# Kernel optimization log

Measured on AMD Instinct MI355X. Metric: run time of the kernel, lower is better.

## Reference

```python
import jax, jax.numpy as jnp
import numpy as np

NUM_DAYOFWEEK, NUM_TIME, NUM_MONTH, NUM_DAY = 7, 24, 12, 31
NUM_DESTINATION = 100000
NUM_FACTOR = 128
NUM_DIM = NUM_FACTOR // 4  # 32
N = 1048576


def setup_inputs() -> dict:
    key = jax.random.key(0)
    ks = jax.random.split(key, 10)
    std = 0.1
    return {
        "dayofweek": jax.random.randint(ks[0], (N,), 0, NUM_DAYOFWEEK),
        "time": jax.random.randint(ks[1], (N,), 0, NUM_TIME),
        "month": jax.random.randint(ks[2], (N,), 0, NUM_MONTH),
        "day": jax.random.randint(ks[3], (N,), 0, NUM_DAY),
        "destination": jax.random.randint(ks[4], (N,), 0, NUM_DESTINATION),
        "W_dayofweek": std * jax.random.normal(ks[5], (NUM_DAYOFWEEK, NUM_DIM), dtype=jnp.float32),
        "W_time": std * jax.random.normal(ks[6], (NUM_TIME, NUM_DIM), dtype=jnp.float32),
        "W_month": std * jax.random.normal(ks[7], (NUM_MONTH, NUM_DIM), dtype=jnp.float32),
        "W_day": std * jax.random.normal(ks[8], (NUM_DAY, NUM_DIM), dtype=jnp.float32),
        "W_item": std * jax.random.normal(ks[9], (NUM_DESTINATION, NUM_FACTOR), dtype=jnp.float32),
    }


def reference(dayofweek, time, month, day, destination,
              W_dayofweek, W_time, W_month, W_day, W_item) -> jnp.ndarray:
    # Gather per-feature embeddings and concat into user vector [N, num_factor]
    user = jnp.concatenate([
        W_dayofweek[dayofweek],  # [N, 32]
        W_time[time],            # [N, 32]
        W_month[month],          # [N, 32]
        W_day[day],              # [N, 32]
    ], axis=-1)
    item = W_item[destination]   # [N, 128]
    # Original: diagonal(mm(user, item.T)) == rowwise dot product; compute it directly.
    return jnp.sum(user * item, axis=-1)  # [N]
```

## Files before the change

kernel.cpp:

```cpp
#include <hip/hip_runtime.h>


typedef unsigned long long u64;

constexpr int NDIM = 32;
constexpr int SZ_DOW = 7 * NDIM, SZ_TIM = 24 * NDIM, SZ_MON = 12 * NDIM, SZ_DAY = 31 * NDIM;
constexpr int B_DOW = 0;
constexpr int B_TIM = B_DOW + SZ_DOW;
constexpr int B_MON = B_TIM + SZ_TIM;
constexpr int B_DAY = B_MON + SZ_MON;
constexpr int TAB_TOT = B_DAY + SZ_DAY;

constexpr int NB     = 32;
constexpr int DDIV   = 3125;
constexpr int SLICES = 256;
constexpr int SPB    = 4096;
constexpr int BIN_T  = 1024;
constexpr int IPT    = SPB / BIN_T;

__device__ __forceinline__ unsigned short f2bf(float f) {
    const unsigned u = __float_as_uint(f);
    return (unsigned short)((u + 0x7FFFu + ((u >> 16) & 1u)) >> 16);
}

__device__ __forceinline__ float dot8bf(uint4 a, float4 u0, float4 u1) {
    float s;
    s  = __uint_as_float(a.x << 16)          * u0.x;
    s += __uint_as_float(a.x & 0xFFFF0000u)  * u0.y;
    s += __uint_as_float(a.y << 16)          * u0.z;
    s += __uint_as_float(a.y & 0xFFFF0000u)  * u0.w;
    s += __uint_as_float(a.z << 16)          * u1.x;
    s += __uint_as_float(a.z & 0xFFFF0000u)  * u1.y;
    s += __uint_as_float(a.w << 16)          * u1.z;
    s += __uint_as_float(a.w & 0xFFFF0000u)  * u1.w;
    return s;
}

__device__ __forceinline__ void load_tab(float* tab, const float* Wdow, const float* Wtim,
                                         const float* Wmon, const float* Wday, int nthr) {
    const int t = threadIdx.x;
    for (int i = t; i < SZ_DOW; i += nthr) tab[B_DOW + i] = Wdow[i];
    for (int i = t; i < SZ_TIM; i += nthr) tab[B_TIM + i] = Wtim[i];
    for (int i = t; i < SZ_MON; i += nthr) tab[B_MON + i] = Wmon[i];
    for (int i = t; i < SZ_DAY; i += nthr) tab[B_DAY + i] = Wday[i];
}

__global__ __launch_bounds__(BIN_T)
void prep_kernel(const int* __restrict__ dow, const int* __restrict__ tim,
                 const int* __restrict__ mon, const int* __restrict__ day,
                 const int* __restrict__ dest,
                 int* __restrict__ cntG, int* __restrict__ lbaseG,
                 u64* __restrict__ payload, int n,
                 const float* __restrict__ Witem, unsigned short* __restrict__ Wb,
                 int witem_elems)
{
    __shared__ u64 stage[SPB];
    __shared__ int hist[NB], lbase[NB], cursor[NB];

    const int t = threadIdx.x, b = blockIdx.x;
    const int g0 = b * SPB;
    const int rem = n - g0;
    const int len = rem < SPB ? rem : SPB;

    int dreg[IPT], pkreg[IPT];
#pragma unroll
    for (int i = 0; i < IPT; i++) {
        const int k = i * BIN_T + t;
        if (k < len) {
            const int idx = g0 + k;
            dreg[i]  = dest[idx];
            pkreg[i] = dow[idx] | (tim[idx] << 3) | (mon[idx] << 8) | (day[idx] << 12);
        } else { dreg[i] = -1; pkreg[i] = 0; }
    }

    if (Wb) {
        const int nf4   = witem_elems >> 2;
        const int chunk = (nf4 + SLICES - 1) / SLICES;
        const int c0    = b * chunk;
        const int c1    = min(c0 + chunk, nf4);
        const float4* src = (const float4*)Witem;
        ushort4* dst = (ushort4*)Wb;
        for (int i = c0 + t; i < c1; i += BIN_T) {
            const float4 v = src[i];
            ushort4 o;
            o.x = f2bf(v.x); o.y = f2bf(v.y); o.z = f2bf(v.z); o.w = f2bf(v.w);
            dst[i] = o;
        }
    }

    if (t < NB) hist[t] = 0;
    __syncthreads();
#pragma unroll
    for (int i = 0; i < IPT; i++)
        if (dreg[i] >= 0) atomicAdd(&hist[dreg[i] / DDIV], 1);
    __syncthreads();
    if (t == 0) {
        int run = 0;
        for (int q = 0; q < NB; q++) { lbase[q] = run; run += hist[q]; }
    }
    __syncthreads();
    if (t < NB) { cursor[t] = lbase[t]; cntG[b * NB + t] = hist[t]; lbaseG[b * NB + t] = lbase[t]; }
    __syncthreads();
#pragma unroll
    for (int i = 0; i < IPT; i++) {
        const int k = i * BIN_T + t;
        if (k < len) {
            const int j = atomicAdd(&cursor[dreg[i] / DDIV], 1);
            stage[j] = (u64)(unsigned)(g0 + k)
                     | ((u64)(unsigned)dreg[i]  << 20)
                     | ((u64)(unsigned)pkreg[i] << 37);
        }
    }
    __syncthreads();
#pragma unroll
    for (int i = 0; i < IPT; i++) {
        const int k = i * BIN_T + t;
        if (k < len) payload[g0 + k] = stage[k];
    }
}

__global__ __launch_bounds__(256, 8)
void mf_main_bf16(const u64* __restrict__ payload,
                  const float* __restrict__ Wdow, const float* __restrict__ Wtim,
                  const float* __restrict__ Wmon, const float* __restrict__ Wday,
                  const unsigned short* __restrict__ Wb,
                  const int* __restrict__ cntG, const int* __restrict__ lbaseG,
                  float* __restrict__ out)
{
    __shared__ float tab[TAB_TOT];
    load_tab(tab, Wdow, Wtim, Wmon, Wday, 256);
    __syncthreads();

    const int tid = threadIdx.x;
    const int sub = tid & 63;
    const int wv  = tid >> 6;
    const int g   = sub >> 3;
    const int l8  = sub & 7;
    const int jt   = l8 >> 1;
    const int half = (l8 & 1) * 16;
    const int tbj  = (jt == 0) ? B_DOW : (jt == 1) ? B_TIM : (jt == 2) ? B_MON : B_DAY;
    const int shj  = (jt == 0) ? 37    : (jt == 1) ? 40    : (jt == 2) ? 45    : 49;
    const int mkj  = (jt == 0) ? 7     : (jt == 1) ? 31    : (jt == 2) ? 15    : 31;

    const int x = blockIdx.x & 7;
    const int s = blockIdx.x >> 3;

    for (int p = 0; p < 4; p++) {
        const int q  = x + 8 * p;
        const int L  = cntG[s * NB + q];
        const int st = s * SPB + lbaseG[s * NB + q];

        int i = wv * 16;
        u64 p0 = (i + g < L)     ? payload[st + i + g]     : 0ull;
        u64 p1 = (i + 8 + g < L) ? payload[st + i + 8 + g] : 0ull;

        for (; i < L; i += 64) {
            const bool v0 = (i + g) < L, v1 = (i + 8 + g) < L;
            const u64 c0 = p0, c1 = p1;
            const int ni = i + 64;
            p0 = (ni + g < L)     ? payload[st + ni + g]     : 0ull;
            p1 = (ni + 8 + g < L) ? payload[st + ni + 8 + g] : 0ull;

            const int d0 = (int)((c0 >> 20) & 0x1FFFFull);
            const int d1 = (int)((c1 >> 20) & 0x1FFFFull);

            const uint4* r0 = (const uint4*)(Wb + (long)d0 * 128 + (l8 << 4));
            const uint4* r1 = (const uint4*)(Wb + (long)d1 * 128 + (l8 << 4));
            const uint4 A0 = r0[0], B0 = r0[1];
            const uint4 A1 = r1[0], B1 = r1[1];

            const int ix0 = (int)((c0 >> shj) & (u64)mkj);
            const int ix1 = (int)((c1 >> shj) & (u64)mkj);
            const float* u0p = &tab[tbj + ix0 * NDIM + half];
            const float* u1p = &tab[tbj + ix1 * NDIM + half];
            const float4 u00 = *(const float4*)(u0p);
            const float4 u01 = *(const float4*)(u0p + 4);
            const float4 u02 = *(const float4*)(u0p + 8);
            const float4 u03 = *(const float4*)(u0p + 12);
            const float4 u10 = *(const float4*)(u1p);
            const float4 u11 = *(const float4*)(u1p + 4);
            const float4 u12 = *(const float4*)(u1p + 8);
            const float4 u13 = *(const float4*)(u1p + 12);

            float a0 = dot8bf(A0, u00, u01) + dot8bf(B0, u02, u03);
            float a1 = dot8bf(A1, u10, u11) + dot8bf(B1, u12, u13);

            a0 += __shfl_xor(a0, 1);  a1 += __shfl_xor(a1, 1);
            a0 += __shfl_xor(a0, 2);  a1 += __shfl_xor(a1, 2);
            a0 += __shfl_xor(a0, 4);  a1 += __shfl_xor(a1, 4);

            if (l8 == 0) {
                if (v0) out[(int)(c0 & 0xFFFFFull)] = a0;
                if (v1) out[(int)(c1 & 0xFFFFFull)] = a1;
            }
        }
    }
}

__global__ __launch_bounds__(256, 8)
void mf_main_f32(const u64* __restrict__ payload,
                 const float* __restrict__ Wdow, const float* __restrict__ Wtim,
                 const float* __restrict__ Wmon, const float* __restrict__ Wday,
                 const float* __restrict__ Witem,
                 const int* __restrict__ cntG, const int* __restrict__ lbaseG,
                 float* __restrict__ out)
{
    __shared__ float tab[TAB_TOT];
    load_tab(tab, Wdow, Wtim, Wmon, Wday, 256);
    __syncthreads();
    const int tid = threadIdx.x;
    const int sub = tid & 63;
    const int wv  = tid >> 6;
    const int g   = sub >> 3;
    const int l8  = sub & 7;
    const int col = l8 * 4;
    const int tb[4] = {B_DOW, B_TIM, B_MON, B_DAY};
    const int sh[4] = {37, 40, 45, 49};
    const int mk[4] = {7, 31, 15, 31};
    const int x = blockIdx.x & 7;
    const int s = blockIdx.x >> 3;
    for (int p = 0; p < 4; p++) {
        const int q  = x + 8 * p;
        const int L  = cntG[s * NB + q];
        const int st = s * SPB + lbaseG[s * NB + q];
        for (int i = wv * 16; i < L; i += 64) {
            const int i0 = i + g, i1 = i + 8 + g;
            const bool v0 = i0 < L, v1 = i1 < L;
            const u64 p0 = v0 ? payload[st + i0] : 0ull;
            const u64 p1 = v1 ? payload[st + i1] : 0ull;
            const int d0 = (int)((p0 >> 20) & 0x1FFFFull);
            const int d1 = (int)((p1 >> 20) & 0x1FFFFull);
            const float* r0 = Witem + (long)d0 * 128 + col;
            const float* r1 = Witem + (long)d1 * 128 + col;
            float4 it0[4], it1[4], us0[4], us1[4];
#pragma unroll
            for (int j = 0; j < 4; j++) it0[j] = *reinterpret_cast<const float4*>(r0 + j * NDIM);
#pragma unroll
            for (int j = 0; j < 4; j++) it1[j] = *reinterpret_cast<const float4*>(r1 + j * NDIM);
#pragma unroll
            for (int j = 0; j < 4; j++) {
                const int idx = (int)((p0 >> sh[j]) & (u64)mk[j]);
                us0[j] = *reinterpret_cast<const float4*>(&tab[tb[j] + idx * NDIM + col]);
            }
#pragma unroll
            for (int j = 0; j < 4; j++) {
                const int idx = (int)((p1 >> sh[j]) & (u64)mk[j]);
                us1[j] = *reinterpret_cast<const float4*>(&tab[tb[j] + idx * NDIM + col]);
            }
            float a0 = 0.f, a1 = 0.f;
#pragma unroll
            for (int j = 0; j < 4; j++) {
                a0 += it0[j].x * us0[j].x + it0[j].y * us0[j].y
                    + it0[j].z * us0[j].z + it0[j].w * us0[j].w;
                a1 += it1[j].x * us1[j].x + it1[j].y * us1[j].y
                    + it1[j].z * us1[j].z + it1[j].w * us1[j].w;
            }
            a0 += __shfl_xor(a0, 1);  a1 += __shfl_xor(a1, 1);
            a0 += __shfl_xor(a0, 2);  a1 += __shfl_xor(a1, 2);
            a0 += __shfl_xor(a0, 4);  a1 += __shfl_xor(a1, 4);
            if (l8 == 0) {
                if (v0) out[(int)(p0 & 0xFFFFFull)] = a0;
                if (v1) out[(int)(p1 & 0xFFFFFull)] = a1;
            }
        }
    }
}

__global__ __launch_bounds__(256, 8)
void mf_dot_kernel(const int* __restrict__ dow, const int* __restrict__ tim,
                   const int* __restrict__ mon, const int* __restrict__ day,
                   const int* __restrict__ dest,
                   const float* __restrict__ Wdow, const float* __restrict__ Wtim,
                   const float* __restrict__ Wmon, const float* __restrict__ Wday,
                   const float* __restrict__ Witem,
                   float* __restrict__ out, int n_samples)
{
    __shared__ float tab[TAB_TOT];
    load_tab(tab, Wdow, Wtim, Wmon, Wday, 256);
    __syncthreads();
    const int tid = threadIdx.x;
    const int lane = tid & 63, sub = lane & 31, wave = tid >> 6, half = lane >> 5;
    const int t = sub >> 3, dofs = (sub & 7) * 4;
    const int* idxp  = (t == 0) ? dow   : (t == 1) ? tim   : (t == 2) ? mon   : day;
    const int  tbase = (t == 0) ? B_DOW : (t == 1) ? B_TIM : (t == 2) ? B_MON : B_DAY;
    long n = (long)blockIdx.x * 8 + wave * 2 + half;
    const long stride = (long)gridDim.x * 8;
    for (; n < n_samples; n += stride) {
        const int idx = idxp[n];
        const int ds  = dest[n];
        const float4 u  = *reinterpret_cast<const float4*>(&tab[tbase + idx * NDIM + dofs]);
        const float4 it = *reinterpret_cast<const float4*>(&Witem[(long)ds * 128 + sub * 4]);
        float r = u.x * it.x + u.y * it.y + u.z * it.z + u.w * it.w;
        r += __shfl_xor(r, 16); r += __shfl_xor(r, 8); r += __shfl_xor(r, 4);
        r += __shfl_xor(r, 2);  r += __shfl_xor(r, 1);
        if (sub == 0) out[n] = r;
    }
}

extern "C" void kernel_launch(void* const* d_in, const int* in_sizes, int n_in,
                              void* d_out, int out_size, void* d_ws, size_t ws_size,
                              hipStream_t stream)
{
    const int*   dow   = (const int*)d_in[0];
    const int*   tim   = (const int*)d_in[1];
    const int*   mon   = (const int*)d_in[2];
    const int*   day   = (const int*)d_in[3];
    const int*   dest  = (const int*)d_in[4];
    const float* Wdow  = (const float*)d_in[5];
    const float* Wtim  = (const float*)d_in[6];
    const float* Wmon  = (const float*)d_in[7];
    const float* Wday  = (const float*)d_in[8];
    const float* Witem = (const float*)d_in[9];
    float* out = (float*)d_out;

    const int n  = in_sizes[0];
    const int we = in_sizes[9];
    const int cap = SLICES * SPB;

    const size_t off_wb       = 64 * 1024;
    const size_t off_pay_full = (off_wb + (size_t)we * 2 + 255) & ~(size_t)255;
    const size_t need_full    = off_pay_full + (size_t)cap * 8;
    const size_t off_pay_mid  = 64 * 1024;
    const size_t need_mid     = off_pay_mid + (size_t)cap * 8;

    if ((size_t)ws_size < need_mid || n > cap) {
        hipLaunchKernelGGL(mf_dot_kernel, dim3(2048), dim3(256), 0, stream,
                           dow, tim, mon, day, dest,
                           Wdow, Wtim, Wmon, Wday, Witem, out, n);
        return;
    }

    const bool full = (size_t)ws_size >= need_full;

    int* cntG   = (int*)d_ws;
    int* lbaseG = (int*)((char*)d_ws + 32 * 1024);
    unsigned short* Wb = full ? (unsigned short*)((char*)d_ws + off_wb) : nullptr;
    u64* payload = (u64*)((char*)d_ws + (full ? off_pay_full : off_pay_mid));

    hipLaunchKernelGGL(prep_kernel, dim3(SLICES), dim3(BIN_T), 0, stream,
                       dow, tim, mon, day, dest, cntG, lbaseG, payload, n,
                       Witem, Wb, we);
    if (full)
        hipLaunchKernelGGL(mf_main_bf16, dim3(SLICES * 8), dim3(256), 0, stream,
                           payload, Wdow, Wtim, Wmon, Wday, Wb, cntG, lbaseG, out);
    else
        hipLaunchKernelGGL(mf_main_f32, dim3(SLICES * 8), dim3(256), 0, stream,
                           payload, Wdow, Wtim, Wmon, Wday, Witem, cntG, lbaseG, out);
}
```

Before: 150.9 us.

## Drop bf16 item-table conversion, use fp32 gather with finer destination bins

Removes the per-call conversion of the whole 100000x128 item table to bf16 and reads fp32 item rows directly in the main kernel. That conversion read 51MB and wrote 25MB on every call. The price is doubled bytes per gathered item row. Destination bins go from 32 to 64 for better cache locality of each block's slice of the item table. Other changes: a wave shuffle scan replaces the serial prefix sum, count and base are packed into one int2 read before the table load, and embedding rows are padded to a 36-float stride to spread shared-memory banks.

```diff
diff --git a/kernel.cpp b/kernel.cpp
--- a/kernel.cpp
+++ b/kernel.cpp
@@ -3,59 +3,39 @@
 
 typedef unsigned long long u64;
 
-constexpr int NDIM = 32;
-constexpr int SZ_DOW = 7 * NDIM, SZ_TIM = 24 * NDIM, SZ_MON = 12 * NDIM, SZ_DAY = 31 * NDIM;
+constexpr int NDIM    = 32;
+constexpr int RSTRIDE = 36;
 constexpr int B_DOW = 0;
-constexpr int B_TIM = B_DOW + SZ_DOW;
-constexpr int B_MON = B_TIM + SZ_TIM;
-constexpr int B_DAY = B_MON + SZ_MON;
-constexpr int TAB_TOT = B_DAY + SZ_DAY;
-
-constexpr int NB     = 32;
-constexpr int DDIV   = 3125;
+constexpr int B_TIM = B_DOW + 7  * RSTRIDE;
+constexpr int B_MON = B_TIM + 24 * RSTRIDE;
+constexpr int B_DAY = B_MON + 12 * RSTRIDE;
+constexpr int TAB_TOT = B_DAY + 31 * RSTRIDE;
+
+constexpr int NB     = 64;
+constexpr int DDIV   = 1563;
 constexpr int SLICES = 256;
 constexpr int SPB    = 4096;
 constexpr int BIN_T  = 1024;
 constexpr int IPT    = SPB / BIN_T;
 
-__device__ __forceinline__ unsigned short f2bf(float f) {
-    const unsigned u = __float_as_uint(f);
-    return (unsigned short)((u + 0x7FFFu + ((u >> 16) & 1u)) >> 16);
-}
-
-__device__ __forceinline__ float dot8bf(uint4 a, float4 u0, float4 u1) {
-    float s;
-    s  = __uint_as_float(a.x << 16)          * u0.x;
-    s += __uint_as_float(a.x & 0xFFFF0000u)  * u0.y;
-    s += __uint_as_float(a.y << 16)          * u0.z;
-    s += __uint_as_float(a.y & 0xFFFF0000u)  * u0.w;
-    s += __uint_as_float(a.z << 16)          * u1.x;
-    s += __uint_as_float(a.z & 0xFFFF0000u)  * u1.y;
-    s += __uint_as_float(a.w << 16)          * u1.z;
-    s += __uint_as_float(a.w & 0xFFFF0000u)  * u1.w;
-    return s;
-}
-
 __device__ __forceinline__ void load_tab(float* tab, const float* Wdow, const float* Wtim,
                                          const float* Wmon, const float* Wday, int nthr) {
     const int t = threadIdx.x;
-    for (int i = t; i < SZ_DOW; i += nthr) tab[B_DOW + i] = Wdow[i];
-    for (int i = t; i < SZ_TIM; i += nthr) tab[B_TIM + i] = Wtim[i];
-    for (int i = t; i < SZ_MON; i += nthr) tab[B_MON + i] = Wmon[i];
-    for (int i = t; i < SZ_DAY; i += nthr) tab[B_DAY + i] = Wday[i];
+    for (int i = t; i < 7  * NDIM; i += nthr) tab[B_DOW + (i >> 5) * RSTRIDE + (i & 31)] = Wdow[i];
+    for (int i = t; i < 24 * NDIM; i += nthr) tab[B_TIM + (i >> 5) * RSTRIDE + (i & 31)] = Wtim[i];
+    for (int i = t; i < 12 * NDIM; i += nthr) tab[B_MON + (i >> 5) * RSTRIDE + (i & 31)] = Wmon[i];
+    for (int i = t; i < 31 * NDIM; i += nthr) tab[B_DAY + (i >> 5) * RSTRIDE + (i & 31)] = Wday[i];
 }
 
 __global__ __launch_bounds__(BIN_T)
 void prep_kernel(const int* __restrict__ dow, const int* __restrict__ tim,
                  const int* __restrict__ mon, const int* __restrict__ day,
                  const int* __restrict__ dest,
-                 int* __restrict__ cntG, int* __restrict__ lbaseG,
-                 u64* __restrict__ payload, int n,
-                 const float* __restrict__ Witem, unsigned short* __restrict__ Wb,
-                 int witem_elems)
+                 int2* __restrict__ clG,
+                 u64* __restrict__ payload, int n)
 {
     __shared__ u64 stage[SPB];
-    __shared__ int hist[NB], lbase[NB], cursor[NB];
+    __shared__ int hist[NB], cursor[NB];
 
     const int t = threadIdx.x, b = blockIdx.x;
     const int g0 = b * SPB;
@@ -73,33 +53,23 @@
         } else { dreg[i] = -1; pkreg[i] = 0; }
     }
 
-    if (Wb) {
-        const int nf4   = witem_elems >> 2;
-        const int chunk = (nf4 + SLICES - 1) / SLICES;
-        const int c0    = b * chunk;
-        const int c1    = min(c0 + chunk, nf4);
-        const float4* src = (const float4*)Witem;
-        ushort4* dst = (ushort4*)Wb;
-        for (int i = c0 + t; i < c1; i += BIN_T) {
-            const float4 v = src[i];
-            ushort4 o;
-            o.x = f2bf(v.x); o.y = f2bf(v.y); o.z = f2bf(v.z); o.w = f2bf(v.w);
-            dst[i] = o;
-        }
-    }
-
     if (t < NB) hist[t] = 0;
     __syncthreads();
 #pragma unroll
     for (int i = 0; i < IPT; i++)
         if (dreg[i] >= 0) atomicAdd(&hist[dreg[i] / DDIV], 1);
     __syncthreads();
-    if (t == 0) {
-        int run = 0;
-        for (int q = 0; q < NB; q++) { lbase[q] = run; run += hist[q]; }
-    }
-    __syncthreads();
-    if (t < NB) { cursor[t] = lbase[t]; cntG[b * NB + t] = hist[t]; lbaseG[b * NB + t] = lbase[t]; }
+    if (t < 64) {
+        int v = hist[t];
+#pragma unroll
+        for (int d = 1; d < 64; d <<= 1) {
+            const int nv = __shfl_up(v, d);
+            if (t >= d) v += nv;
+        }
+        const int base = v - hist[t];
+        cursor[t] = base;
+        clG[b * NB + t] = make_int2(hist[t], base);
+    }
     __syncthreads();
 #pragma unroll
     for (int i = 0; i < IPT; i++) {
@@ -119,96 +89,27 @@
     }
 }
 
-__global__ __launch_bounds__(256, 8)
-void mf_main_bf16(const u64* __restrict__ payload,
-                  const float* __restrict__ Wdow, const float* __restrict__ Wtim,
-                  const float* __restrict__ Wmon, const float* __restrict__ Wday,
-                  const unsigned short* __restrict__ Wb,
-                  const int* __restrict__ cntG, const int* __restrict__ lbaseG,
-                  float* __restrict__ out)
+__global__ __launch_bounds__(256, 4)
+void mf_main(const u64* __restrict__ payload,
+             const float* __restrict__ Wdow, const float* __restrict__ Wtim,
+             const float* __restrict__ Wmon, const float* __restrict__ Wday,
+             const float* __restrict__ Witem,
+             const int2* __restrict__ clG,
+             float* __restrict__ out)
 {
     __shared__ float tab[TAB_TOT];
-    load_tab(tab, Wdow, Wtim, Wmon, Wday, 256);
-    __syncthreads();
 
     const int tid = threadIdx.x;
-    const int sub = tid & 63;
-    const int wv  = tid >> 6;
-    const int g   = sub >> 3;
-    const int l8  = sub & 7;
-    const int jt   = l8 >> 1;
-    const int half = (l8 & 1) * 16;
-    const int tbj  = (jt == 0) ? B_DOW : (jt == 1) ? B_TIM : (jt == 2) ? B_MON : B_DAY;
-    const int shj  = (jt == 0) ? 37    : (jt == 1) ? 40    : (jt == 2) ? 45    : 49;
-    const int mkj  = (jt == 0) ? 7     : (jt == 1) ? 31    : (jt == 2) ? 15    : 31;
-
     const int x = blockIdx.x & 7;
     const int s = blockIdx.x >> 3;
 
-    for (int p = 0; p < 4; p++) {
-        const int q  = x + 8 * p;
-        const int L  = cntG[s * NB + q];
-        const int st = s * SPB + lbaseG[s * NB + q];
-
-        int i = wv * 16;
-        u64 p0 = (i + g < L)     ? payload[st + i + g]     : 0ull;
-        u64 p1 = (i + 8 + g < L) ? payload[st + i + 8 + g] : 0ull;
-
-        for (; i < L; i += 64) {
-            const bool v0 = (i + g) < L, v1 = (i + 8 + g) < L;
-            const u64 c0 = p0, c1 = p1;
-            const int ni = i + 64;
-            p0 = (ni + g < L)     ? payload[st + ni + g]     : 0ull;
-            p1 = (ni + 8 + g < L) ? payload[st + ni + 8 + g] : 0ull;
-
-            const int d0 = (int)((c0 >> 20) & 0x1FFFFull);
-            const int d1 = (int)((c1 >> 20) & 0x1FFFFull);
-
-            const uint4* r0 = (const uint4*)(Wb + (long)d0 * 128 + (l8 << 4));
-            const uint4* r1 = (const uint4*)(Wb + (long)d1 * 128 + (l8 << 4));
-            const uint4 A0 = r0[0], B0 = r0[1];
-            const uint4 A1 = r1[0], B1 = r1[1];
-
-            const int ix0 = (int)((c0 >> shj) & (u64)mkj);
-            const int ix1 = (int)((c1 >> shj) & (u64)mkj);
-            const float* u0p = &tab[tbj + ix0 * NDIM + half];
-            const float* u1p = &tab[tbj + ix1 * NDIM + half];
-            const float4 u00 = *(const float4*)(u0p);
-            const float4 u01 = *(const float4*)(u0p + 4);
-            const float4 u02 = *(const float4*)(u0p + 8);
-            const float4 u03 = *(const float4*)(u0p + 12);
-            const float4 u10 = *(const float4*)(u1p);
-            const float4 u11 = *(const float4*)(u1p + 4);
-            const float4 u12 = *(const float4*)(u1p + 8);
-            const float4 u13 = *(const float4*)(u1p + 12);
-
-            float a0 = dot8bf(A0, u00, u01) + dot8bf(B0, u02, u03);
-            float a1 = dot8bf(A1, u10, u11) + dot8bf(B1, u12, u13);
-
-            a0 += __shfl_xor(a0, 1);  a1 += __shfl_xor(a1, 1);
-            a0 += __shfl_xor(a0, 2);  a1 += __shfl_xor(a1, 2);
-            a0 += __shfl_xor(a0, 4);  a1 += __shfl_xor(a1, 4);
-
-            if (l8 == 0) {
-                if (v0) out[(int)(c0 & 0xFFFFFull)] = a0;
-                if (v1) out[(int)(c1 & 0xFFFFFull)] = a1;
-            }
-        }
-    }
-}
-
-__global__ __launch_bounds__(256, 8)
-void mf_main_f32(const u64* __restrict__ payload,
-                 const float* __restrict__ Wdow, const float* __restrict__ Wtim,
-                 const float* __restrict__ Wmon, const float* __restrict__ Wday,
-                 const float* __restrict__ Witem,
-                 const int* __restrict__ cntG, const int* __restrict__ lbaseG,
-                 float* __restrict__ out)
-{
-    __shared__ float tab[TAB_TOT];
+    int2 cl[8];
+#pragma unroll
+    for (int p = 0; p < 8; p++) cl[p] = clG[s * NB + x + 8 * p];
+
     load_tab(tab, Wdow, Wtim, Wmon, Wday, 256);
     __syncthreads();
-    const int tid = threadIdx.x;
+
     const int sub = tid & 63;
     const int wv  = tid >> 6;
     const int g   = sub >> 3;
@@ -217,12 +118,10 @@
     const int tb[4] = {B_DOW, B_TIM, B_MON, B_DAY};
     const int sh[4] = {37, 40, 45, 49};
     const int mk[4] = {7, 31, 15, 31};
-    const int x = blockIdx.x & 7;
-    const int s = blockIdx.x >> 3;
-    for (int p = 0; p < 4; p++) {
-        const int q  = x + 8 * p;
-        const int L  = cntG[s * NB + q];
-        const int st = s * SPB + lbaseG[s * NB + q];
+
+    for (int p = 0; p < 8; p++) {
+        const int L  = cl[p].x;
+        const int st = s * SPB + cl[p].y;
         for (int i = wv * 16; i < L; i += 64) {
             const int i0 = i + g, i1 = i + 8 + g;
             const bool v0 = i0 < L, v1 = i1 < L;
@@ -240,12 +139,12 @@
 #pragma unroll
             for (int j = 0; j < 4; j++) {
                 const int idx = (int)((p0 >> sh[j]) & (u64)mk[j]);
-                us0[j] = *reinterpret_cast<const float4*>(&tab[tb[j] + idx * NDIM + col]);
+                us0[j] = *reinterpret_cast<const float4*>(&tab[tb[j] + idx * RSTRIDE + col]);
             }
 #pragma unroll
             for (int j = 0; j < 4; j++) {
                 const int idx = (int)((p1 >> sh[j]) & (u64)mk[j]);
-                us1[j] = *reinterpret_cast<const float4*>(&tab[tb[j] + idx * NDIM + col]);
+                us1[j] = *reinterpret_cast<const float4*>(&tab[tb[j] + idx * RSTRIDE + col]);
             }
             float a0 = 0.f, a1 = 0.f;
 #pragma unroll
@@ -288,7 +187,7 @@
     for (; n < n_samples; n += stride) {
         const int idx = idxp[n];
         const int ds  = dest[n];
-        const float4 u  = *reinterpret_cast<const float4*>(&tab[tbase + idx * NDIM + dofs]);
+        const float4 u  = *reinterpret_cast<const float4*>(&tab[tbase + idx * RSTRIDE + dofs]);
         const float4 it = *reinterpret_cast<const float4*>(&Witem[(long)ds * 128 + sub * 4]);
         float r = u.x * it.x + u.y * it.y + u.z * it.z + u.w * it.w;
         r += __shfl_xor(r, 16); r += __shfl_xor(r, 8); r += __shfl_xor(r, 4);
@@ -313,37 +212,24 @@
     const float* Witem = (const float*)d_in[9];
     float* out = (float*)d_out;
 
-    const int n  = in_sizes[0];
-    const int we = in_sizes[9];
+    const int n   = in_sizes[0];
     const int cap = SLICES * SPB;
 
-    const size_t off_wb       = 64 * 1024;
-    const size_t off_pay_full = (off_wb + (size_t)we * 2 + 255) & ~(size_t)255;
-    const size_t need_full    = off_pay_full + (size_t)cap * 8;
-    const size_t off_pay_mid  = 64 * 1024;
-    const size_t need_mid     = off_pay_mid + (size_t)cap * 8;
-
-    if ((size_t)ws_size < need_mid || n > cap) {
+    const size_t off_pay = 128 * 1024;
+    const size_t need    = off_pay + (size_t)cap * 8;
+
+    if ((size_t)ws_size < need || n > cap) {
         hipLaunchKernelGGL(mf_dot_kernel, dim3(2048), dim3(256), 0, stream,
                            dow, tim, mon, day, dest,
                            Wdow, Wtim, Wmon, Wday, Witem, out, n);
         return;
     }
 
-    const bool full = (size_t)ws_size >= need_full;
-
-    int* cntG   = (int*)d_ws;
-    int* lbaseG = (int*)((char*)d_ws + 32 * 1024);
-    unsigned short* Wb = full ? (unsigned short*)((char*)d_ws + off_wb) : nullptr;
-    u64* payload = (u64*)((char*)d_ws + (full ? off_pay_full : off_pay_mid));
+    int2* clG    = (int2*)d_ws;
+    u64* payload = (u64*)((char*)d_ws + off_pay);
 
     hipLaunchKernelGGL(prep_kernel, dim3(SLICES), dim3(BIN_T), 0, stream,
-                       dow, tim, mon, day, dest, cntG, lbaseG, payload, n,
-                       Witem, Wb, we);
-    if (full)
-        hipLaunchKernelGGL(mf_main_bf16, dim3(SLICES * 8), dim3(256), 0, stream,
-                           payload, Wdow, Wtim, Wmon, Wday, Wb, cntG, lbaseG, out);
-    else
-        hipLaunchKernelGGL(mf_main_f32, dim3(SLICES * 8), dim3(256), 0, stream,
-                           payload, Wdow, Wtim, Wmon, Wday, Witem, cntG, lbaseG, out);
-}
+                       dow, tim, mon, day, dest, clG, payload, n);
+    hipLaunchKernelGGL(mf_main, dim3(SLICES * 8), dim3(256), 0, stream,
+                       payload, Wdow, Wtim, Wmon, Wday, Witem, clG, out);
+}
```

Result: slower. 164.5 us (+9.0%).
